# Performance work log

Hardware: AMD Instinct MI355X
Metric: run time of the kernel (lower is better)

Reference implementation:

```python
import jax, jax.numpy as jnp
import numpy as np

N, E = 50000, 150000
IN, HID, LAT, EF, HE = 16, 32, 16, 8, 128


def _p(k, shape, fan_in):
    return jax.random.normal(k, shape, jnp.float32) / np.float32(np.sqrt(fan_in))


def setup_inputs() -> dict:
    key = jax.random.key(0)
    ks = jax.random.split(key, 32)
    inp = {
        "x": jax.random.normal(ks[0], (N, IN), jnp.float32),
        "edge_index": jax.random.randint(ks[1], (2, E), 0, N, dtype=jnp.int64),
        "edge_attr": jax.random.uniform(ks[2], (E, EF), jnp.float32),
    }
    # per-conv params: edge-MLP (w1,b1,w2,b2), root weight, bias
    dims = {"c1": (IN, HID), "c2": (HID, HID), "cmu": (HID, LAT), "clv": (HID, LAT)}
    i = 3
    for name, (din, dout) in dims.items():
        inp[f"{name}_w1"] = _p(ks[i], (EF, HE), EF)
        inp[f"{name}_b1"] = jnp.zeros((HE,), jnp.float32)
        inp[f"{name}_w2"] = _p(ks[i + 1], (HE, din * dout), HE)
        inp[f"{name}_b2"] = jnp.zeros((din * dout,), jnp.float32)
        inp[f"{name}_root"] = _p(ks[i + 2], (din, dout), din)
        inp[f"{name}_bias"] = jnp.zeros((dout,), jnp.float32)
        i += 3
    return inp


def _nnconv(x, src, dst, ea, w1, b1, w2, b2, root, bias, din, dout, mean):
    # edge MLP -> per-edge weight matrix [E, din, dout]
    h = jax.nn.relu(ea @ w1 + b1)
    W = (h @ w2 + b2).reshape(-1, din, dout)
    # gather source features, per-edge matmul, scatter-reduce to targets
    msg = jnp.einsum('ei,eio->eo', x[src], W)  # [E, dout]
    agg = jax.ops.segment_sum(msg, dst, num_segments=x.shape[0])
    if mean:
        cnt = jax.ops.segment_sum(jnp.ones((dst.shape[0],), x.dtype), dst,
                                  num_segments=x.shape[0])
        agg = agg / jnp.maximum(cnt, 1.0)[:, None]
    return agg + x @ root + bias


def reference(x, edge_index, edge_attr,
              c1_w1, c1_b1, c1_w2, c1_b2, c1_root, c1_bias,
              c2_w1, c2_b1, c2_w2, c2_b2, c2_root, c2_bias,
              cmu_w1, cmu_b1, cmu_w2, cmu_b2, cmu_root, cmu_bias,
              clv_w1, clv_b1, clv_w2, clv_b2, clv_root, clv_bias):
    src, dst = edge_index[0], edge_index[1]
    h = jax.nn.relu(_nnconv(x, src, dst, edge_attr, c1_w1, c1_b1, c1_w2, c1_b2,
                            c1_root, c1_bias, IN, HID, True))
    h = jax.nn.relu(_nnconv(h, src, dst, edge_attr, c2_w1, c2_b1, c2_w2, c2_b2,
                            c2_root, c2_bias, HID, HID, True))
    mu = _nnconv(h, src, dst, edge_attr, cmu_w1, cmu_b1, cmu_w2, cmu_b2,
                 cmu_root, cmu_bias, HID, LAT, False)
    logvar = _nnconv(h, src, dst, edge_attr, clv_w1, clv_b1, clv_w2, clv_b2,
                     clv_root, clv_bias, HID, LAT, False)
    return mu, logvar
```

## Files before the change

kernel.cpp:

```cpp
#include <hip/hip_runtime.h>

typedef __attribute__((ext_vector_type(8))) _Float16 half8;
typedef __attribute__((ext_vector_type(4))) _Float16 half4v;
typedef __attribute__((ext_vector_type(2))) _Float16 half2v;
typedef __attribute__((ext_vector_type(4))) float f32x4;

constexpr int NN  = 50000;
constexpr int NE  = 150000;
constexpr int IN  = 16;
constexpr int HID = 32;
constexpr int LAT = 16;
constexpr int EF  = 8;
constexpr int HE  = 128;
constexpr int NTILE = NE / 16;
constexpr int HSTR  = HE + 2;

constexpr int SCB = 256;
constexpr int NSB = (NN + SCB - 1) / SCB;

union XU {
  half2v h2[4];
  half8  h8;
  _Float16 h[8];
};

__global__ void count_kernel(const int* __restrict__ dst, int* __restrict__ cnt) {
  int e = blockIdx.x * blockDim.x + threadIdx.x;
  if (e < NE) atomicAdd(&cnt[dst[e]], 1);
}

__launch_bounds__(SCB)
__global__ void scan1(const int* __restrict__ cnt, int* __restrict__ bsum) {
  __shared__ int sdata[SCB];
  const int i = blockIdx.x * SCB + threadIdx.x;
  sdata[threadIdx.x] = (i < NN) ? cnt[i] : 0;
  __syncthreads();
  for (int off = SCB / 2; off > 0; off >>= 1) {
    if (threadIdx.x < off) sdata[threadIdx.x] += sdata[threadIdx.x + off];
    __syncthreads();
  }
  if (threadIdx.x == 0) bsum[blockIdx.x] = sdata[0];
}

__launch_bounds__(SCB)
__global__ void scan2(int* __restrict__ bsum) {
  __shared__ int sdata[SCB];
  const int t = threadIdx.x;
  const int v = (t < NSB) ? bsum[t] : 0;
  sdata[t] = v;
  __syncthreads();
  for (int off = 1; off < SCB; off <<= 1) {
    int u = (t >= off) ? sdata[t - off] : 0;
    __syncthreads();
    sdata[t] += u;
    __syncthreads();
  }
  if (t < NSB) bsum[t] = sdata[t] - v;
}

__launch_bounds__(SCB)
__global__ void scan3(const int* __restrict__ cnt, const int* __restrict__ bsum,
                      int* __restrict__ rowptr, int* __restrict__ wptr) {
  __shared__ int sdata[SCB];
  const int i = blockIdx.x * SCB + threadIdx.x;
  const int t = threadIdx.x;
  const int v = (i < NN) ? cnt[i] : 0;
  sdata[t] = v;
  __syncthreads();
  for (int off = 1; off < SCB; off <<= 1) {
    int u = (t >= off) ? sdata[t - off] : 0;
    __syncthreads();
    sdata[t] += u;
    __syncthreads();
  }
  const int excl = sdata[t] - v + bsum[blockIdx.x];
  if (i < NN) {
    rowptr[i] = excl;
    wptr[i]   = excl;
  }
  if (i == NN - 1) rowptr[NN] = NE;
}

__global__ void fill_kernel(const int* __restrict__ dst, int* __restrict__ wptr,
                            int* __restrict__ epos) {
  int e = blockIdx.x * blockDim.x + threadIdx.x;
  if (e < NE) epos[e] = atomicAdd(&wptr[dst[e]], 1);
}

__global__ void swizzle_kernel(const float* __restrict__ w2, const float* __restrict__ b2,
                               const float* __restrict__ w1,
                               _Float16* __restrict__ w2h, float* __restrict__ w1t,
                               int DIN_, int DOUT_) {
  int idx = blockIdx.x * blockDim.x + threadIdx.x;
  if (idx < HE * EF) {
    int kk = idx / EF, i = idx % EF;
    w1t[idx] = w1[i * HE + kk];
  }
  int tot = HSTR * DIN_ * DOUT_;
  if (idx >= tot) return;
  int i  = idx % DIN_;
  int o  = (idx / DIN_) % DOUT_;
  int kk = idx / (DIN_ * DOUT_);
  float v = 0.0f;
  if (kk < HE)       v = w2[(size_t)kk * DIN_ * DOUT_ + i * DOUT_ + o];
  else if (kk == HE) v = b2[i * DOUT_ + o];
  w2h[idx] = (_Float16)v;
}

template <int DIN, int DOUT, bool DUAL>
__launch_bounds__(128)
__global__ void nnconv_mfma(const float* __restrict__ xin,
                            const int*   __restrict__ src,
                            const float* __restrict__ ea,
                            const float* __restrict__ w1tA,
                            const float* __restrict__ b1A,
                            const float* __restrict__ w1tB,
                            const float* __restrict__ b1B,
                            const _Float16* __restrict__ w2hA,
                            const _Float16* __restrict__ w2hB,
                            const int*   __restrict__ epos,
                            _Float16* __restrict__ msgA,
                            _Float16* __restrict__ msgB)
{
  constexpr int KKSTEP  = 32 / DIN;
  constexpr int CHS     = 8 / KKSTEP;
  constexpr int BSTRIDE = KKSTEP * DOUT * DIN;
  constexpr int HS      = 136;
  constexpr int TILES   = 4;

  __shared__ _Float16 h_s[128 * HS];

  const int tid = threadIdx.x;
  const int eb  = blockIdx.x * 128;

  float eav[EF];
  {
    const int e = eb + tid;
    float4 v0 = make_float4(0.f, 0.f, 0.f, 0.f), v1 = v0;
    if (e < NE) {
      const float4* p = (const float4*)(ea + (size_t)e * EF);
      v0 = p[0]; v1 = p[1];
    }
    eav[0] = v0.x; eav[1] = v0.y; eav[2] = v0.z; eav[3] = v0.w;
    eav[4] = v1.x; eav[5] = v1.y; eav[6] = v1.z; eav[7] = v1.w;
  }

  auto build_h = [&](const float* __restrict__ w1t, const float* __restrict__ b1) {
#pragma unroll 1
    for (int c = 0; c < 16; c++) {
      const float4 bq0 = *(const float4*)&b1[c * 8];
      const float4 bq1 = *(const float4*)&b1[c * 8 + 4];
      const float bk[8] = {bq0.x, bq0.y, bq0.z, bq0.w, bq1.x, bq1.y, bq1.z, bq1.w};
      XU hr;
#pragma unroll
      for (int j = 0; j < 8; j++) {
        const int kk = c * 8 + j;
        const float4 wa = *(const float4*)&w1t[kk * EF];
        const float4 wb = *(const float4*)&w1t[kk * EF + 4];
        float hv = bk[j];
        hv = fmaf(eav[0], wa.x, hv); hv = fmaf(eav[1], wa.y, hv);
        hv = fmaf(eav[2], wa.z, hv); hv = fmaf(eav[3], wa.w, hv);
        hv = fmaf(eav[4], wb.x, hv); hv = fmaf(eav[5], wb.y, hv);
        hv = fmaf(eav[6], wb.z, hv); hv = fmaf(eav[7], wb.w, hv);
        hv = fmaxf(hv, 0.0f);
        hr.h[j] = (_Float16)hv;
      }
      *(half8*)&h_s[tid * HS + c * 8] = hr.h8;
    }
  };

  build_h(w1tA, b1A);
  __syncthreads();

  const int wave = tid >> 6;
  const int lane = tid & 63;
  const int m = lane & 15, q = lane >> 4;
  const int i0 = (q * 8) % DIN;
  const int kq = (q * 8) / DIN;
  const int tg0 = blockIdx.x * 8 + wave * TILES;

  XU xv[TILES];
#pragma unroll
  for (int t = 0; t < TILES; t++) {
    const int tg = tg0 + t;
    if (tg < NTILE) {
      const int s = src[tg * 16 + m];
      const float4* xp = (const float4*)(xin + (size_t)s * DIN + i0);
      const float4 a = xp[0], b = xp[1];
      xv[t].h2[0] = (half2v){(_Float16)a.x, (_Float16)a.y};
      xv[t].h2[1] = (half2v){(_Float16)a.z, (_Float16)a.w};
      xv[t].h2[2] = (half2v){(_Float16)b.x, (_Float16)b.y};
      xv[t].h2[3] = (half2v){(_Float16)b.z, (_Float16)b.w};
    } else {
#pragma unroll
      for (int j = 0; j < 4; j++) xv[t].h2[j] = (half2v){(_Float16)0.f, (_Float16)0.f};
    }
  }

  f32x4 acc[TILES][2];
#pragma unroll
  for (int t = 0; t < TILES; t++)
#pragma unroll
    for (int f = 0; f < 2; f++) acc[t][f] = (f32x4){0.f, 0.f, 0.f, 0.f};

  int hrow[TILES];
#pragma unroll
  for (int t = 0; t < TILES; t++) hrow[t] = wave * 64 + t * 16 + m;

  auto make_af = [&](const XU& xvt, _Float16 hv) -> XU {
    const half2v hb = (half2v){hv, hv};
    XU af;
#pragma unroll
    for (int j = 0; j < 4; j++) af.h2[j] = xvt.h2[j] * hb;
    return af;
  };

  if constexpr (DUAL) {
    auto run_pass = [&](const _Float16* __restrict__ bp, const int f) {
#pragma unroll 1
      for (int c = 0; c < 16; c++) {
        XU hc[TILES];
#pragma unroll
        for (int t = 0; t < TILES; t++)
          hc[t].h8 = *(const half8*)&h_s[hrow[t] * HS + c * 8];
#pragma unroll
        for (int s = 0; s < CHS; s++) {
          const half8 bf = *(const half8*)(bp + (size_t)(c * CHS + s) * BSTRIDE);
#pragma unroll
          for (int t = 0; t < TILES; t++) {
            _Float16 hv;
            if (DIN == 32) hv = hc[t].h[s];
            else {
              const _Float16 h0 = hc[t].h[2 * s], h1 = hc[t].h[2 * s + 1];
              hv = kq ? h1 : h0;
            }
            const XU af = make_af(xv[t], hv);
            acc[t][f] = __builtin_amdgcn_mfma_f32_16x16x32_f16(af.h8, bf,
                                                               acc[t][f], 0, 0, 0);
          }
        }
      }
      {
        const half8 bf = *(const half8*)(bp + (size_t)(128 / KKSTEP) * BSTRIDE);
#pragma unroll
        for (int t = 0; t < TILES; t++) {
          XU af;
          if (DIN == 32) af = xv[t];
          else {
#pragma unroll
            for (int j = 0; j < 4; j++)
              af.h2[j] = kq ? (half2v){(_Float16)0.f, (_Float16)0.f} : xv[t].h2[j];
          }
          acc[t][f] = __builtin_amdgcn_mfma_f32_16x16x32_f16(af.h8, bf,
                                                             acc[t][f], 0, 0, 0);
        }
      }
    };

    const _Float16* bpA = w2hA + (size_t)(kq * DOUT + m) * DIN + i0;
    const _Float16* bpB = w2hB + (size_t)(kq * DOUT + m) * DIN + i0;
    run_pass(bpA, 0);
    __syncthreads();
    build_h(w1tB, b1B);
    __syncthreads();
    run_pass(bpB, 1);
  } else {
    const _Float16* bp0 = w2hA + (size_t)(kq * DOUT + 0 + m) * DIN + i0;
    const _Float16* bp1 = w2hA + (size_t)(kq * DOUT + 16 + m) * DIN + i0;
#pragma unroll 1
    for (int c = 0; c < 16; c++) {
      XU hc[TILES];
#pragma unroll
      for (int t = 0; t < TILES; t++)
        hc[t].h8 = *(const half8*)&h_s[hrow[t] * HS + c * 8];
#pragma unroll
      for (int s = 0; s < CHS; s++) {
        const half8 bf0 = *(const half8*)(bp0 + (size_t)(c * CHS + s) * BSTRIDE);
        const half8 bf1 = *(const half8*)(bp1 + (size_t)(c * CHS + s) * BSTRIDE);
#pragma unroll
        for (int t = 0; t < TILES; t++) {
          _Float16 hv;
          if (DIN == 32) hv = hc[t].h[s];
          else {
            const _Float16 h0 = hc[t].h[2 * s], h1 = hc[t].h[2 * s + 1];
            hv = kq ? h1 : h0;
          }
          const XU af = make_af(xv[t], hv);
          acc[t][0] = __builtin_amdgcn_mfma_f32_16x16x32_f16(af.h8, bf0,
                                                             acc[t][0], 0, 0, 0);
          acc[t][1] = __builtin_amdgcn_mfma_f32_16x16x32_f16(af.h8, bf1,
                                                             acc[t][1], 0, 0, 0);
        }
      }
    }
    {
      const half8 bf0 = *(const half8*)(bp0 + (size_t)(128 / KKSTEP) * BSTRIDE);
      const half8 bf1 = *(const half8*)(bp1 + (size_t)(128 / KKSTEP) * BSTRIDE);
#pragma unroll
      for (int t = 0; t < TILES; t++) {
        XU af;
        if (DIN == 32) af = xv[t];
        else {
#pragma unroll
          for (int j = 0; j < 4; j++)
            af.h2[j] = kq ? (half2v){(_Float16)0.f, (_Float16)0.f} : xv[t].h2[j];
        }
        acc[t][0] = __builtin_amdgcn_mfma_f32_16x16x32_f16(af.h8, bf0,
                                                           acc[t][0], 0, 0, 0);
        acc[t][1] = __builtin_amdgcn_mfma_f32_16x16x32_f16(af.h8, bf1,
                                                           acc[t][1], 0, 0, 0);
      }
    }
  }

#pragma unroll
  for (int t = 0; t < TILES; t++) {
    const int tg = tg0 + t;
    if (tg < NTILE) {
      const int ebase = tg * 16 + q * 4;
      const int4 ep = *(const int4*)(epos + ebase);
      const int pr[4] = {ep.x, ep.y, ep.z, ep.w};
      if (DUAL) {
#pragma unroll
        for (int r = 0; r < 4; r++) {
          msgA[(size_t)pr[r] * DOUT + m] = (_Float16)acc[t][0][r];
          msgB[(size_t)pr[r] * DOUT + m] = (_Float16)acc[t][1][r];
        }
      } else {
#pragma unroll
        for (int f = 0; f < 2; f++)
#pragma unroll
          for (int r = 0; r < 4; r++)
            msgA[(size_t)pr[r] * DOUT + f * 16 + m] = (_Float16)acc[t][f][r];
      }
    }
  }
}

template <int DIN, int DOUT, bool MEAN, bool RELU>
__launch_bounds__(256)
__global__ void finish_kernel(const _Float16* __restrict__ msg,
                              const int* __restrict__ rowptr,
                              const float* __restrict__ xin,
                              const float* __restrict__ root,
                              const float* __restrict__ bias,
                              float* __restrict__ out) {
  constexpr int TPN = DOUT / 4;
  const int gid = blockIdx.x * 256 + threadIdx.x;
  const int n = gid / TPN, sub = gid % TPN;
  if (n >= NN) return;
  const int o0 = sub * 4;

  const int r0 = rowptr[n], r1 = rowptr[n + 1];
  float ax = 0.f, ay = 0.f, az = 0.f, aw = 0.f;
  for (int idx = r0; idx < r1; idx++) {
    const half4v mv = *(const half4v*)(msg + (size_t)idx * DOUT + o0);
    ax += (float)mv.x; ay += (float)mv.y; az += (float)mv.z; aw += (float)mv.w;
  }
  const float inv = MEAN ? 1.0f / fmaxf((float)(r1 - r0), 1.0f) : 1.0f;
  float vx = ax * inv + bias[o0 + 0];
  float vy = ay * inv + bias[o0 + 1];
  float vz = az * inv + bias[o0 + 2];
  float vw = aw * inv + bias[o0 + 3];
#pragma unroll
  for (int i = 0; i < DIN; i++) {
    const float xi = xin[(size_t)n * DIN + i];
    const float4 rv = *(const float4*)(root + (size_t)i * DOUT + o0);
    vx = fmaf(xi, rv.x, vx); vy = fmaf(xi, rv.y, vy);
    vz = fmaf(xi, rv.z, vz); vw = fmaf(xi, rv.w, vw);
  }
  if (RELU) {
    vx = fmaxf(vx, 0.f); vy = fmaxf(vy, 0.f);
    vz = fmaxf(vz, 0.f); vw = fmaxf(vw, 0.f);
  }
  *(float4*)(out + (size_t)n * DOUT + o0) = make_float4(vx, vy, vz, vw);
}

template <int DIN>
__launch_bounds__(256)
__global__ void finish_dual(const _Float16* __restrict__ msgA,
                            const _Float16* __restrict__ msgB,
                            const int* __restrict__ rowptr,
                            const float* __restrict__ xin,
                            const float* __restrict__ rootA,
                            const float* __restrict__ biasA,
                            const float* __restrict__ rootB,
                            const float* __restrict__ biasB,
                            float* __restrict__ outA,
                            float* __restrict__ outB) {
  constexpr int TPN = LAT / 4;
  const int gid = blockIdx.x * 256 + threadIdx.x;
  const int n = gid / TPN, sub = gid % TPN;
  if (n >= NN) return;
  const int o0 = sub * 4;

  const int r0 = rowptr[n], r1 = rowptr[n + 1];
  float a0 = 0.f, a1 = 0.f, a2 = 0.f, a3 = 0.f;
  float b0 = 0.f, b1 = 0.f, b2 = 0.f, b3 = 0.f;
  for (int idx = r0; idx < r1; idx++) {
    const half4v ma = *(const half4v*)(msgA + (size_t)idx * LAT + o0);
    const half4v mb = *(const half4v*)(msgB + (size_t)idx * LAT + o0);
    a0 += (float)ma.x; a1 += (float)ma.y; a2 += (float)ma.z; a3 += (float)ma.w;
    b0 += (float)mb.x; b1 += (float)mb.y; b2 += (float)mb.z; b3 += (float)mb.w;
  }
  float va0 = a0 + biasA[o0 + 0], va1 = a1 + biasA[o0 + 1];
  float va2 = a2 + biasA[o0 + 2], va3 = a3 + biasA[o0 + 3];
  float vb0 = b0 + biasB[o0 + 0], vb1 = b1 + biasB[o0 + 1];
  float vb2 = b2 + biasB[o0 + 2], vb3 = b3 + biasB[o0 + 3];
#pragma unroll
  for (int i = 0; i < DIN; i++) {
    const float xi = xin[(size_t)n * DIN + i];
    const float4 ra = *(const float4*)(rootA + (size_t)i * LAT + o0);
    const float4 rb = *(const float4*)(rootB + (size_t)i * LAT + o0);
    va0 = fmaf(xi, ra.x, va0); va1 = fmaf(xi, ra.y, va1);
    va2 = fmaf(xi, ra.z, va2); va3 = fmaf(xi, ra.w, va3);
    vb0 = fmaf(xi, rb.x, vb0); vb1 = fmaf(xi, rb.y, vb1);
    vb2 = fmaf(xi, rb.z, vb2); vb3 = fmaf(xi, rb.w, vb3);
  }
  *(float4*)(outA + (size_t)n * LAT + o0) = make_float4(va0, va1, va2, va3);
  *(float4*)(outB + (size_t)n * LAT + o0) = make_float4(vb0, vb1, vb2, vb3);
}

extern "C" void kernel_launch(void* const* d_in, const int* in_sizes, int n_in,
                              void* d_out, int out_size, void* d_ws, size_t ws_size,
                              hipStream_t stream) {
  const float* x  = (const float*)d_in[0];
  const int*   ei = (const int*)d_in[1];
  const float* ea = (const float*)d_in[2];
  const int* src = ei;
  const int* dst = ei + NE;

  auto P = [&](int c, int j) -> const float* {
    return (const float*)d_in[3 + c * 6 + j];
  };

  float* h1  = (float*)d_ws;
  float* h2  = h1 + (size_t)NN * HID;
  _Float16* msg = (_Float16*)(h2 + (size_t)NN * HID);
  int* cnt    = (int*)(msg + (size_t)NE * 32);
  int* rowptr = cnt + NN;
  int* wptr   = rowptr + 50004;
  int* epos   = wptr + 50004;
  int* bsum   = epos + NE;
  _Float16* w2h_c1 = (_Float16*)(bsum + 256);
  _Float16* w2h_c2 = w2h_c1 + (size_t)HSTR * 32 * 16;
  _Float16* w2h_mu = w2h_c2 + (size_t)HSTR * 32 * 32;
  _Float16* w2h_lv = w2h_mu + (size_t)HSTR * 16 * 32;
  float* w1t_c1 = (float*)(w2h_lv + (size_t)HSTR * 16 * 32);
  float* w1t_c2 = w1t_c1 + HE * EF;
  float* w1t_mu = w1t_c2 + HE * EF;
  float* w1t_lv = w1t_mu + HE * EF;

  _Float16* msgA = msg;
  _Float16* msgB = msg + (size_t)NE * 16;

  float* out_mu = (float*)d_out;
  float* out_lv = out_mu + (size_t)NN * LAT;

  hipMemsetAsync(cnt, 0, (size_t)NN * sizeof(int), stream);
  count_kernel<<<dim3((NE + 255) / 256), dim3(256), 0, stream>>>(dst, cnt);
  scan1<<<dim3(NSB), dim3(SCB), 0, stream>>>(cnt, bsum);
  scan2<<<dim3(1), dim3(SCB), 0, stream>>>(bsum);
  scan3<<<dim3(NSB), dim3(SCB), 0, stream>>>(cnt, bsum, rowptr, wptr);
  fill_kernel<<<dim3((NE + 255) / 256), dim3(256), 0, stream>>>(dst, wptr, epos);

  {
    int t1 = HSTR * 16 * 32, t2 = HSTR * 32 * 32, t3 = HSTR * 32 * 16;
    swizzle_kernel<<<dim3((t1 + 255) / 256), dim3(256), 0, stream>>>(
        P(0, 2), P(0, 3), P(0, 0), w2h_c1, w1t_c1, IN, HID);
    swizzle_kernel<<<dim3((t2 + 255) / 256), dim3(256), 0, stream>>>(
        P(1, 2), P(1, 3), P(1, 0), w2h_c2, w1t_c2, HID, HID);
    swizzle_kernel<<<dim3((t3 + 255) / 256), dim3(256), 0, stream>>>(
        P(2, 2), P(2, 3), P(2, 0), w2h_mu, w1t_mu, HID, LAT);
    swizzle_kernel<<<dim3((t3 + 255) / 256), dim3(256), 0, stream>>>(
        P(3, 2), P(3, 3), P(3, 0), w2h_lv, w1t_lv, HID, LAT);
  }

  const dim3 egrid((NTILE + 7) / 8), eblk(128);

  nnconv_mfma<IN, HID, false><<<egrid, eblk, 0, stream>>>(
      x, src, ea, w1t_c1, P(0, 1), nullptr, nullptr, w2h_c1, nullptr,
      epos, msg, nullptr);
  finish_kernel<IN, HID, true, true>
      <<<dim3((NN * (HID / 4) + 255) / 256), dim3(256), 0, stream>>>(
          msg, rowptr, x, P(0, 4), P(0, 5), h1);

  nnconv_mfma<HID, HID, false><<<egrid, eblk, 0, stream>>>(
      h1, src, ea, w1t_c2, P(1, 1), nullptr, nullptr, w2h_c2, nullptr,
      epos, msg, nullptr);
  finish_kernel<HID, HID, true, true>
      <<<dim3((NN * (HID / 4) + 255) / 256), dim3(256), 0, stream>>>(
          msg, rowptr, h1, P(1, 4), P(1, 5), h2);

  nnconv_mfma<HID, LAT, true><<<egrid, eblk, 0, stream>>>(
      h2, src, ea, w1t_mu, P(2, 1), w1t_lv, P(3, 1), w2h_mu, w2h_lv,
      epos, msgA, msgB);
  finish_dual<HID>
      <<<dim3((NN * (LAT / 4) + 255) / 256), dim3(256), 0, stream>>>(
          msgA, msgB, rowptr, h2, P(2, 4), P(2, 5), P(3, 4), P(3, 5),
          out_mu, out_lv);
}
```

Before: 361.6 us.

## Split dual mu/logvar conv across waves instead of sequential passes

In the dual (mu/logvar) NNConv kernel, each 128-thread block now handles 64 edges, with wave 0 computing the mu branch and wave 1 the logvar branch at the same time. Before, both waves ran the mu pass, then a barrier, a rebuild of the hidden edge-MLP activations, another barrier, and the logvar pass. The change drops the mid-kernel barriers and the serial second build_h, and doubles the grid. The cost is that each edge's attributes and source features are loaded by both waves, and each wave now builds h for only 64 edges, which leaves half the LDS buffer unused.

```diff
diff --git a/kernel.cpp b/kernel.cpp
--- a/kernel.cpp
+++ b/kernel.cpp
@@ -127,15 +127,18 @@
   constexpr int BSTRIDE = KKSTEP * DOUT * DIN;
   constexpr int HS      = 136;
   constexpr int TILES   = 4;
+  constexpr int EDGES   = DUAL ? 64 : 128;
 
   __shared__ _Float16 h_s[128 * HS];
 
-  const int tid = threadIdx.x;
-  const int eb  = blockIdx.x * 128;
+  const int tid  = threadIdx.x;
+  const int wave = tid >> 6;
+  const int lane = tid & 63;
+  const int eb   = blockIdx.x * EDGES;
 
   float eav[EF];
   {
-    const int e = eb + tid;
+    const int e = eb + (DUAL ? lane : tid);
     float4 v0 = make_float4(0.f, 0.f, 0.f, 0.f), v1 = v0;
     if (e < NE) {
       const float4* p = (const float4*)(ea + (size_t)e * EF);
@@ -169,15 +172,18 @@
     }
   };
 
-  build_h(w1tA, b1A);
+  if constexpr (DUAL) {
+    build_h(wave == 0 ? w1tA : w1tB, wave == 0 ? b1A : b1B);
+  } else {
+    build_h(w1tA, b1A);
+  }
   __syncthreads();
 
-  const int wave = tid >> 6;
-  const int lane = tid & 63;
   const int m = lane & 15, q = lane >> 4;
   const int i0 = (q * 8) % DIN;
   const int kq = (q * 8) / DIN;
-  const int tg0 = blockIdx.x * 8 + wave * TILES;
+  const int tg0 = DUAL ? blockIdx.x * TILES
+                       : blockIdx.x * (2 * TILES) + wave * TILES;
 
   XU xv[TILES];
 #pragma unroll
@@ -197,12 +203,6 @@
     }
   }
 
-  f32x4 acc[TILES][2];
-#pragma unroll
-  for (int t = 0; t < TILES; t++)
-#pragma unroll
-    for (int f = 0; f < 2; f++) acc[t][f] = (f32x4){0.f, 0.f, 0.f, 0.f};
-
   int hrow[TILES];
 #pragma unroll
   for (int t = 0; t < TILES; t++) hrow[t] = wave * 64 + t * 16 + m;
@@ -216,55 +216,72 @@
   };
 
   if constexpr (DUAL) {
-    auto run_pass = [&](const _Float16* __restrict__ bp, const int f) {
+    f32x4 acc[TILES];
+#pragma unroll
+    for (int t = 0; t < TILES; t++) acc[t] = (f32x4){0.f, 0.f, 0.f, 0.f};
+
+    const _Float16* base = (wave == 0) ? w2hA : w2hB;
+    const _Float16* bp = base + (size_t)(kq * DOUT + m) * DIN + i0;
+
 #pragma unroll 1
-      for (int c = 0; c < 16; c++) {
-        XU hc[TILES];
-#pragma unroll
-        for (int t = 0; t < TILES; t++)
-          hc[t].h8 = *(const half8*)&h_s[hrow[t] * HS + c * 8];
-#pragma unroll
-        for (int s = 0; s < CHS; s++) {
-          const half8 bf = *(const half8*)(bp + (size_t)(c * CHS + s) * BSTRIDE);
-#pragma unroll
-          for (int t = 0; t < TILES; t++) {
-            _Float16 hv;
-            if (DIN == 32) hv = hc[t].h[s];
-            else {
-              const _Float16 h0 = hc[t].h[2 * s], h1 = hc[t].h[2 * s + 1];
-              hv = kq ? h1 : h0;
-            }
-            const XU af = make_af(xv[t], hv);
-            acc[t][f] = __builtin_amdgcn_mfma_f32_16x16x32_f16(af.h8, bf,
-                                                               acc[t][f], 0, 0, 0);
+    for (int c = 0; c < 16; c++) {
+      XU hc[TILES];
+#pragma unroll
+      for (int t = 0; t < TILES; t++)
+        hc[t].h8 = *(const half8*)&h_s[hrow[t] * HS + c * 8];
+#pragma unroll
+      for (int s = 0; s < CHS; s++) {
+        const half8 bf = *(const half8*)(bp + (size_t)(c * CHS + s) * BSTRIDE);
+#pragma unroll
+        for (int t = 0; t < TILES; t++) {
+          _Float16 hv;
+          if (DIN == 32) hv = hc[t].h[s];
+          else {
+            const _Float16 h0 = hc[t].h[2 * s], h1 = hc[t].h[2 * s + 1];
+            hv = kq ? h1 : h0;
           }
+          const XU af = make_af(xv[t], hv);
+          acc[t] = __builtin_amdgcn_mfma_f32_16x16x32_f16(af.h8, bf,
+                                                          acc[t], 0, 0, 0);
         }
       }
-      {
-        const half8 bf = *(const half8*)(bp + (size_t)(128 / KKSTEP) * BSTRIDE);
-#pragma unroll
-        for (int t = 0; t < TILES; t++) {
-          XU af;
-          if (DIN == 32) af = xv[t];
-          else {
-#pragma unroll
-            for (int j = 0; j < 4; j++)
-              af.h2[j] = kq ? (half2v){(_Float16)0.f, (_Float16)0.f} : xv[t].h2[j];
-          }
-          acc[t][f] = __builtin_amdgcn_mfma_f32_16x16x32_f16(af.h8, bf,
-                                                             acc[t][f], 0, 0, 0);
+    }
+    {
+      const half8 bf = *(const half8*)(bp + (size_t)(128 / KKSTEP) * BSTRIDE);
+#pragma unroll
+      for (int t = 0; t < TILES; t++) {
+        XU af;
+        if (DIN == 32) af = xv[t];
+        else {
+#pragma unroll
+          for (int j = 0; j < 4; j++)
+            af.h2[j] = kq ? (half2v){(_Float16)0.f, (_Float16)0.f} : xv[t].h2[j];
         }
-      }
-    };
-
-    const _Float16* bpA = w2hA + (size_t)(kq * DOUT + m) * DIN + i0;
-    const _Float16* bpB = w2hB + (size_t)(kq * DOUT + m) * DIN + i0;
-    run_pass(bpA, 0);
-    __syncthreads();
-    build_h(w1tB, b1B);
-    __syncthreads();
-    run_pass(bpB, 1);
+        acc[t] = __builtin_amdgcn_mfma_f32_16x16x32_f16(af.h8, bf,
+                                                        acc[t], 0, 0, 0);
+      }
+    }
+
+    _Float16* mout = (wave == 0) ? msgA : msgB;
+#pragma unroll
+    for (int t = 0; t < TILES; t++) {
+      const int tg = tg0 + t;
+      if (tg < NTILE) {
+        const int ebase = tg * 16 + q * 4;
+        const int4 ep = *(const int4*)(epos + ebase);
+        const int pr[4] = {ep.x, ep.y, ep.z, ep.w};
+#pragma unroll
+        for (int r = 0; r < 4; r++)
+          mout[(size_t)pr[r] * DOUT + m] = (_Float16)acc[t][r];
+      }
+    }
   } else {
+    f32x4 acc[TILES][2];
+#pragma unroll
+    for (int t = 0; t < TILES; t++)
+#pragma unroll
+      for (int f = 0; f < 2; f++) acc[t][f] = (f32x4){0.f, 0.f, 0.f, 0.f};
+
     const _Float16* bp0 = w2hA + (size_t)(kq * DOUT + 0 + m) * DIN + i0;
     const _Float16* bp1 = w2hA + (size_t)(kq * DOUT + 16 + m) * DIN + i0;
 #pragma unroll 1
@@ -311,22 +328,14 @@
                                                            acc[t][1], 0, 0, 0);
       }
     }
-  }
-
-#pragma unroll
-  for (int t = 0; t < TILES; t++) {
-    const int tg = tg0 + t;
-    if (tg < NTILE) {
-      const int ebase = tg * 16 + q * 4;
-      const int4 ep = *(const int4*)(epos + ebase);
-      const int pr[4] = {ep.x, ep.y, ep.z, ep.w};
-      if (DUAL) {
-#pragma unroll
-        for (int r = 0; r < 4; r++) {
-          msgA[(size_t)pr[r] * DOUT + m] = (_Float16)acc[t][0][r];
-          msgB[(size_t)pr[r] * DOUT + m] = (_Float16)acc[t][1][r];
-        }
-      } else {
+
+#pragma unroll
+    for (int t = 0; t < TILES; t++) {
+      const int tg = tg0 + t;
+      if (tg < NTILE) {
+        const int ebase = tg * 16 + q * 4;
+        const int4 ep = *(const int4*)(epos + ebase);
+        const int pr[4] = {ep.x, ep.y, ep.z, ep.w};
 #pragma unroll
         for (int f = 0; f < 2; f++)
 #pragma unroll
@@ -477,6 +486,7 @@
   }
 
   const dim3 egrid((NTILE + 7) / 8), eblk(128);
+  const dim3 dgrid((NTILE + 3) / 4);
 
   nnconv_mfma<IN, HID, false><<<egrid, eblk, 0, stream>>>(
       x, src, ea, w1t_c1, P(0, 1), nullptr, nullptr, w2h_c1, nullptr,
@@ -492,7 +502,7 @@
       <<<dim3((NN * (HID / 4) + 255) / 256), dim3(256), 0, stream>>>(
           msg, rowptr, h1, P(1, 4), P(1, 5), h2);
 
-  nnconv_mfma<HID, LAT, true><<<egrid, eblk, 0, stream>>>(
+  nnconv_mfma<HID, LAT, true><<<dgrid, eblk, 0, stream>>>(
       h2, src, ea, w1t_mu, P(2, 1), w1t_lv, P(3, 1), w2h_mu, w2h_lv,
       epos, msgA, msgB);
   finish_dual<HID>
```

Result: slower. 379.5 us (+5.0%).

## Split edge-MLP hidden dimension across two blocks with partial message buffers

Applied to the files above, without the earlier changes.

Adds a second grid dimension that splits the 128-wide edge-MLP hidden reduction into two halves, each block building only 64 hidden units in a smaller shared tile and writing its partial messages to a separate buffer. The finish kernels then sum the two partial message buffers while aggregating. This doubles the block count and halves the shared memory per block, aiming at more occupancy and parallelism in the MFMA kernels. In exchange, the edge features and source rows are loaded twice, and the message write and read traffic doubles.

```diff
diff --git a/kernel.cpp b/kernel.cpp
--- a/kernel.cpp
+++ b/kernel.cpp
@@ -125,13 +125,17 @@
   constexpr int KKSTEP  = 32 / DIN;
   constexpr int CHS     = 8 / KKSTEP;
   constexpr int BSTRIDE = KKSTEP * DOUT * DIN;
-  constexpr int HS      = 136;
+  constexpr int HS      = 72;
+  constexpr int CPB     = 8;
   constexpr int TILES   = 4;
 
   __shared__ _Float16 h_s[128 * HS];
 
-  const int tid = threadIdx.x;
-  const int eb  = blockIdx.x * 128;
+  const int tid  = threadIdx.x;
+  const int wave = tid >> 6;
+  const int lane = tid & 63;
+  const int eb   = blockIdx.x * 128;
+  const int yh   = blockIdx.y;
 
   float eav[EF];
   {
@@ -147,14 +151,15 @@
 
   auto build_h = [&](const float* __restrict__ w1t, const float* __restrict__ b1) {
 #pragma unroll 1
-    for (int c = 0; c < 16; c++) {
-      const float4 bq0 = *(const float4*)&b1[c * 8];
-      const float4 bq1 = *(const float4*)&b1[c * 8 + 4];
+    for (int c = 0; c < CPB; c++) {
+      const int kk0 = yh * 64 + c * 8;
+      const float4 bq0 = *(const float4*)&b1[kk0];
+      const float4 bq1 = *(const float4*)&b1[kk0 + 4];
       const float bk[8] = {bq0.x, bq0.y, bq0.z, bq0.w, bq1.x, bq1.y, bq1.z, bq1.w};
       XU hr;
 #pragma unroll
       for (int j = 0; j < 8; j++) {
-        const int kk = c * 8 + j;
+        const int kk = kk0 + j;
         const float4 wa = *(const float4*)&w1t[kk * EF];
         const float4 wb = *(const float4*)&w1t[kk * EF + 4];
         float hv = bk[j];
@@ -172,8 +177,6 @@
   build_h(w1tA, b1A);
   __syncthreads();
 
-  const int wave = tid >> 6;
-  const int lane = tid & 63;
   const int m = lane & 15, q = lane >> 4;
   const int i0 = (q * 8) % DIN;
   const int kq = (q * 8) / DIN;
@@ -197,12 +200,6 @@
     }
   }
 
-  f32x4 acc[TILES][2];
-#pragma unroll
-  for (int t = 0; t < TILES; t++)
-#pragma unroll
-    for (int f = 0; f < 2; f++) acc[t][f] = (f32x4){0.f, 0.f, 0.f, 0.f};
-
   int hrow[TILES];
 #pragma unroll
   for (int t = 0; t < TILES; t++) hrow[t] = wave * 64 + t * 16 + m;
@@ -215,17 +212,26 @@
     return af;
   };
 
+  const int stepbase = yh * CPB * CHS;
+
   if constexpr (DUAL) {
+    f32x4 acc[TILES][2];
+#pragma unroll
+    for (int t = 0; t < TILES; t++)
+#pragma unroll
+      for (int f = 0; f < 2; f++) acc[t][f] = (f32x4){0.f, 0.f, 0.f, 0.f};
+
     auto run_pass = [&](const _Float16* __restrict__ bp, const int f) {
 #pragma unroll 1
-      for (int c = 0; c < 16; c++) {
+      for (int c = 0; c < CPB; c++) {
         XU hc[TILES];
 #pragma unroll
         for (int t = 0; t < TILES; t++)
           hc[t].h8 = *(const half8*)&h_s[hrow[t] * HS + c * 8];
 #pragma unroll
         for (int s = 0; s < CHS; s++) {
-          const half8 bf = *(const half8*)(bp + (size_t)(c * CHS + s) * BSTRIDE);
+          const half8 bf =
+              *(const half8*)(bp + (size_t)(stepbase + c * CHS + s) * BSTRIDE);
 #pragma unroll
           for (int t = 0; t < TILES; t++) {
             _Float16 hv;
@@ -240,7 +246,7 @@
           }
         }
       }
-      {
+      if (yh == 0) {
         const half8 bf = *(const half8*)(bp + (size_t)(128 / KKSTEP) * BSTRIDE);
 #pragma unroll
         for (int t = 0; t < TILES; t++) {
@@ -264,19 +270,44 @@
     build_h(w1tB, b1B);
     __syncthreads();
     run_pass(bpB, 1);
+
+    _Float16* moutA = msgA + (size_t)yh * NE * DOUT;
+    _Float16* moutB = msgB + (size_t)yh * NE * DOUT;
+#pragma unroll
+    for (int t = 0; t < TILES; t++) {
+      const int tg = tg0 + t;
+      if (tg < NTILE) {
+        const int ebase = tg * 16 + q * 4;
+        const int4 ep = *(const int4*)(epos + ebase);
+        const int pr[4] = {ep.x, ep.y, ep.z, ep.w};
+#pragma unroll
+        for (int r = 0; r < 4; r++) {
+          moutA[(size_t)pr[r] * DOUT + m] = (_Float16)acc[t][0][r];
+          moutB[(size_t)pr[r] * DOUT + m] = (_Float16)acc[t][1][r];
+        }
+      }
+    }
   } else {
+    f32x4 acc[TILES][2];
+#pragma unroll
+    for (int t = 0; t < TILES; t++)
+#pragma unroll
+      for (int f = 0; f < 2; f++) acc[t][f] = (f32x4){0.f, 0.f, 0.f, 0.f};
+
     const _Float16* bp0 = w2hA + (size_t)(kq * DOUT + 0 + m) * DIN + i0;
     const _Float16* bp1 = w2hA + (size_t)(kq * DOUT + 16 + m) * DIN + i0;
 #pragma unroll 1
-    for (int c = 0; c < 16; c++) {
+    for (int c = 0; c < CPB; c++) {
       XU hc[TILES];
 #pragma unroll
       for (int t = 0; t < TILES; t++)
         hc[t].h8 = *(const half8*)&h_s[hrow[t] * HS + c * 8];
 #pragma unroll
       for (int s = 0; s < CHS; s++) {
-        const half8 bf0 = *(const half8*)(bp0 + (size_t)(c * CHS + s) * BSTRIDE);
-        const half8 bf1 = *(const half8*)(bp1 + (size_t)(c * CHS + s) * BSTRIDE);
+        const half8 bf0 =
+            *(const half8*)(bp0 + (size_t)(stepbase + c * CHS + s) * BSTRIDE);
+        const half8 bf1 =
+            *(const half8*)(bp1 + (size_t)(stepbase + c * CHS + s) * BSTRIDE);
 #pragma unroll
         for (int t = 0; t < TILES; t++) {
           _Float16 hv;
@@ -293,7 +324,7 @@
         }
       }
     }
-    {
+    if (yh == 0) {
       const half8 bf0 = *(const half8*)(bp0 + (size_t)(128 / KKSTEP) * BSTRIDE);
       const half8 bf1 = *(const half8*)(bp1 + (size_t)(128 / KKSTEP) * BSTRIDE);
 #pragma unroll
@@ -311,27 +342,20 @@
                                                            acc[t][1], 0, 0, 0);
       }
     }
-  }
-
-#pragma unroll
-  for (int t = 0; t < TILES; t++) {
-    const int tg = tg0 + t;
-    if (tg < NTILE) {
-      const int ebase = tg * 16 + q * 4;
-      const int4 ep = *(const int4*)(epos + ebase);
-      const int pr[4] = {ep.x, ep.y, ep.z, ep.w};
-      if (DUAL) {
-#pragma unroll
-        for (int r = 0; r < 4; r++) {
-          msgA[(size_t)pr[r] * DOUT + m] = (_Float16)acc[t][0][r];
-          msgB[(size_t)pr[r] * DOUT + m] = (_Float16)acc[t][1][r];
-        }
-      } else {
+
+    _Float16* mout = msgA + (size_t)yh * NE * DOUT;
+#pragma unroll
+    for (int t = 0; t < TILES; t++) {
+      const int tg = tg0 + t;
+      if (tg < NTILE) {
+        const int ebase = tg * 16 + q * 4;
+        const int4 ep = *(const int4*)(epos + ebase);
+        const int pr[4] = {ep.x, ep.y, ep.z, ep.w};
 #pragma unroll
         for (int f = 0; f < 2; f++)
 #pragma unroll
           for (int r = 0; r < 4; r++)
-            msgA[(size_t)pr[r] * DOUT + f * 16 + m] = (_Float16)acc[t][f][r];
+            mout[(size_t)pr[r] * DOUT + f * 16 + m] = (_Float16)acc[t][f][r];
       }
     }
   }
@@ -350,12 +374,15 @@
   const int n = gid / TPN, sub = gid % TPN;
   if (n >= NN) return;
   const int o0 = sub * 4;
+  const _Float16* msg1 = msg + (size_t)NE * DOUT;
 
   const int r0 = rowptr[n], r1 = rowptr[n + 1];
   float ax = 0.f, ay = 0.f, az = 0.f, aw = 0.f;
   for (int idx = r0; idx < r1; idx++) {
-    const half4v mv = *(const half4v*)(msg + (size_t)idx * DOUT + o0);
-    ax += (float)mv.x; ay += (float)mv.y; az += (float)mv.z; aw += (float)mv.w;
+    const half4v m0 = *(const half4v*)(msg  + (size_t)idx * DOUT + o0);
+    const half4v m1 = *(const half4v*)(msg1 + (size_t)idx * DOUT + o0);
+    ax += (float)m0.x + (float)m1.x; ay += (float)m0.y + (float)m1.y;
+    az += (float)m0.z + (float)m1.z; aw += (float)m0.w + (float)m1.w;
   }
   const float inv = MEAN ? 1.0f / fmaxf((float)(r1 - r0), 1.0f) : 1.0f;
   float vx = ax * inv + bias[o0 + 0];
@@ -393,15 +420,21 @@
   const int n = gid / TPN, sub = gid % TPN;
   if (n >= NN) return;
   const int o0 = sub * 4;
+  const _Float16* msgA1 = msgA + (size_t)NE * LAT;
+  const _Float16* msgB1 = msgB + (size_t)NE * LAT;
 
   const int r0 = rowptr[n], r1 = rowptr[n + 1];
   float a0 = 0.f, a1 = 0.f, a2 = 0.f, a3 = 0.f;
   float b0 = 0.f, b1 = 0.f, b2 = 0.f, b3 = 0.f;
   for (int idx = r0; idx < r1; idx++) {
-    const half4v ma = *(const half4v*)(msgA + (size_t)idx * LAT + o0);
-    const half4v mb = *(const half4v*)(msgB + (size_t)idx * LAT + o0);
-    a0 += (float)ma.x; a1 += (float)ma.y; a2 += (float)ma.z; a3 += (float)ma.w;
-    b0 += (float)mb.x; b1 += (float)mb.y; b2 += (float)mb.z; b3 += (float)mb.w;
+    const half4v ma0 = *(const half4v*)(msgA  + (size_t)idx * LAT + o0);
+    const half4v ma1 = *(const half4v*)(msgA1 + (size_t)idx * LAT + o0);
+    const half4v mb0 = *(const half4v*)(msgB  + (size_t)idx * LAT + o0);
+    const half4v mb1 = *(const half4v*)(msgB1 + (size_t)idx * LAT + o0);
+    a0 += (float)ma0.x + (float)ma1.x; a1 += (float)ma0.y + (float)ma1.y;
+    a2 += (float)ma0.z + (float)ma1.z; a3 += (float)ma0.w + (float)ma1.w;
+    b0 += (float)mb0.x + (float)mb1.x; b1 += (float)mb0.y + (float)mb1.y;
+    b2 += (float)mb0.z + (float)mb1.z; b3 += (float)mb0.w + (float)mb1.w;
   }
   float va0 = a0 + biasA[o0 + 0], va1 = a1 + biasA[o0 + 1];
   float va2 = a2 + biasA[o0 + 2], va3 = a3 + biasA[o0 + 3];
@@ -437,7 +470,7 @@
   float* h1  = (float*)d_ws;
   float* h2  = h1 + (size_t)NN * HID;
   _Float16* msg = (_Float16*)(h2 + (size_t)NN * HID);
-  int* cnt    = (int*)(msg + (size_t)NE * 32);
+  int* cnt    = (int*)(msg + (size_t)NE * 64);
   int* rowptr = cnt + NN;
   int* wptr   = rowptr + 50004;
   int* epos   = wptr + 50004;
@@ -452,7 +485,7 @@
   float* w1t_lv = w1t_mu + HE * EF;
 
   _Float16* msgA = msg;
-  _Float16* msgB = msg + (size_t)NE * 16;
+  _Float16* msgB = msg + (size_t)NE * 32;
 
   float* out_mu = (float*)d_out;
   float* out_lv = out_mu + (size_t)NN * LAT;
@@ -476,21 +509,21 @@
         P(3, 2), P(3, 3), P(3, 0), w2h_lv, w1t_lv, HID, LAT);
   }
 
-  const dim3 egrid((NTILE + 7) / 8), eblk(128);
+  const dim3 egrid((NTILE + 7) / 8, 2), eblk(128);
 
   nnconv_mfma<IN, HID, false><<<egrid, eblk, 0, stream>>>(
       x, src, ea, w1t_c1, P(0, 1), nullptr, nullptr, w2h_c1, nullptr,
-      epos, msg, nullptr);
+      epos, msgA, nullptr);
   finish_kernel<IN, HID, true, true>
       <<<dim3((NN * (HID / 4) + 255) / 256), dim3(256), 0, stream>>>(
-          msg, rowptr, x, P(0, 4), P(0, 5), h1);
+          msgA, rowptr, x, P(0, 4), P(0, 5), h1);
 
   nnconv_mfma<HID, HID, false><<<egrid, eblk, 0, stream>>>(
       h1, src, ea, w1t_c2, P(1, 1), nullptr, nullptr, w2h_c2, nullptr,
-      epos, msg, nullptr);
+      epos, msgA, nullptr);
   finish_kernel<HID, HID, true, true>
       <<<dim3((NN * (HID / 4) + 255) / 256), dim3(256), 0, stream>>>(
-          msg, rowptr, h1, P(1, 4), P(1, 5), h2);
+          msgA, rowptr, h1, P(1, 4), P(1, 5), h2);
 
   nnconv_mfma<HID, LAT, true><<<egrid, eblk, 0, stream>>>(
       h2, src, ea, w1t_mu, P(2, 1), w1t_lv, P(3, 1), w2h_mu, w2h_lv,
```

After: 391.3 us. +8.2%, slower.

## Interleave hidden-activation build with MFMA loop using double-buffered chunk LDS

Applied to the files above, without the earlier changes.

Instead of building the full 128x128 edge-MLP hidden tile in shared memory before the MFMA loop, each 8-wide chunk of hidden units is computed per iteration into a small double-buffered LDS area, and both convs of the dual path are built and consumed in the same loop. This shrinks LDS from about 34KB to a few KB, which could raise occupancy. Interleaving VALU hidden-unit computation with MFMA work lets the two overlap. The cost is one barrier per chunk instead of one or three overall, and the dual path now keeps more live registers because both accumulators and both hidden chunks are active at once.

```diff
diff --git a/kernel.cpp b/kernel.cpp
--- a/kernel.cpp
+++ b/kernel.cpp
@@ -125,13 +125,15 @@
   constexpr int KKSTEP  = 32 / DIN;
   constexpr int CHS     = 8 / KKSTEP;
   constexpr int BSTRIDE = KKSTEP * DOUT * DIN;
-  constexpr int HS      = 136;
   constexpr int TILES   = 4;
-
-  __shared__ _Float16 h_s[128 * HS];
-
-  const int tid = threadIdx.x;
-  const int eb  = blockIdx.x * 128;
+  constexpr int NTAB    = DUAL ? 2 : 1;
+
+  __shared__ _Float16 h_s[2 * NTAB * 128 * 8];
+
+  const int tid  = threadIdx.x;
+  const int wave = tid >> 6;
+  const int lane = tid & 63;
+  const int eb   = blockIdx.x * 128;
 
   float eav[EF];
   {
@@ -145,35 +147,30 @@
     eav[4] = v1.x; eav[5] = v1.y; eav[6] = v1.z; eav[7] = v1.w;
   }
 
-  auto build_h = [&](const float* __restrict__ w1t, const float* __restrict__ b1) {
-#pragma unroll 1
-    for (int c = 0; c < 16; c++) {
-      const float4 bq0 = *(const float4*)&b1[c * 8];
-      const float4 bq1 = *(const float4*)&b1[c * 8 + 4];
-      const float bk[8] = {bq0.x, bq0.y, bq0.z, bq0.w, bq1.x, bq1.y, bq1.z, bq1.w};
-      XU hr;
-#pragma unroll
-      for (int j = 0; j < 8; j++) {
-        const int kk = c * 8 + j;
-        const float4 wa = *(const float4*)&w1t[kk * EF];
-        const float4 wb = *(const float4*)&w1t[kk * EF + 4];
-        float hv = bk[j];
-        hv = fmaf(eav[0], wa.x, hv); hv = fmaf(eav[1], wa.y, hv);
-        hv = fmaf(eav[2], wa.z, hv); hv = fmaf(eav[3], wa.w, hv);
-        hv = fmaf(eav[4], wb.x, hv); hv = fmaf(eav[5], wb.y, hv);
-        hv = fmaf(eav[6], wb.z, hv); hv = fmaf(eav[7], wb.w, hv);
-        hv = fmaxf(hv, 0.0f);
-        hr.h[j] = (_Float16)hv;
-      }
-      *(half8*)&h_s[tid * HS + c * 8] = hr.h8;
-    }
+  auto build_chunk = [&](const float* __restrict__ w1t,
+                         const float* __restrict__ b1,
+                         int c, _Float16* __restrict__ dst) {
+    const int kk0 = c * 8;
+    const float4 bq0 = *(const float4*)&b1[kk0];
+    const float4 bq1 = *(const float4*)&b1[kk0 + 4];
+    const float bk[8] = {bq0.x, bq0.y, bq0.z, bq0.w, bq1.x, bq1.y, bq1.z, bq1.w};
+    XU hr;
+#pragma unroll
+    for (int j = 0; j < 8; j++) {
+      const int kk = kk0 + j;
+      const float4 wa = *(const float4*)&w1t[kk * EF];
+      const float4 wb = *(const float4*)&w1t[kk * EF + 4];
+      float hv = bk[j];
+      hv = fmaf(eav[0], wa.x, hv); hv = fmaf(eav[1], wa.y, hv);
+      hv = fmaf(eav[2], wa.z, hv); hv = fmaf(eav[3], wa.w, hv);
+      hv = fmaf(eav[4], wb.x, hv); hv = fmaf(eav[5], wb.y, hv);
+      hv = fmaf(eav[6], wb.z, hv); hv = fmaf(eav[7], wb.w, hv);
+      hv = fmaxf(hv, 0.0f);
+      hr.h[j] = (_Float16)hv;
+    }
+    *(half8*)&dst[tid * 8] = hr.h8;
   };
 
-  build_h(w1tA, b1A);
-  __syncthreads();
-
-  const int wave = tid >> 6;
-  const int lane = tid & 63;
   const int m = lane & 15, q = lane >> 4;
   const int i0 = (q * 8) % DIN;
   const int kq = (q * 8) / DIN;
@@ -215,101 +212,82 @@
     return af;
   };
 
-  if constexpr (DUAL) {
-    auto run_pass = [&](const _Float16* __restrict__ bp, const int f) {
+  const _Float16* bp0;
+  const _Float16* bp1;
+  if (DUAL) {
+    bp0 = w2hA + (size_t)(kq * DOUT + m) * DIN + i0;
+    bp1 = w2hB + (size_t)(kq * DOUT + m) * DIN + i0;
+  } else {
+    bp0 = w2hA + (size_t)(kq * DOUT + 0 + m) * DIN + i0;
+    bp1 = w2hA + (size_t)(kq * DOUT + 16 + m) * DIN + i0;
+  }
+
 #pragma unroll 1
-      for (int c = 0; c < 16; c++) {
-        XU hc[TILES];
-#pragma unroll
-        for (int t = 0; t < TILES; t++)
-          hc[t].h8 = *(const half8*)&h_s[hrow[t] * HS + c * 8];
-#pragma unroll
-        for (int s = 0; s < CHS; s++) {
-          const half8 bf = *(const half8*)(bp + (size_t)(c * CHS + s) * BSTRIDE);
-#pragma unroll
-          for (int t = 0; t < TILES; t++) {
-            _Float16 hv;
-            if (DIN == 32) hv = hc[t].h[s];
-            else {
-              const _Float16 h0 = hc[t].h[2 * s], h1 = hc[t].h[2 * s + 1];
-              hv = kq ? h1 : h0;
-            }
-            const XU af = make_af(xv[t], hv);
-            acc[t][f] = __builtin_amdgcn_mfma_f32_16x16x32_f16(af.h8, bf,
-                                                               acc[t][f], 0, 0, 0);
+  for (int c = 0; c < 16; c++) {
+    _Float16* buf = &h_s[(size_t)(c & 1) * NTAB * 128 * 8];
+    build_chunk(w1tA, b1A, c, buf);
+    if (DUAL) build_chunk(w1tB, b1B, c, buf + 128 * 8);
+    __syncthreads();
+
+    XU hc0[TILES], hc1[TILES];
+#pragma unroll
+    for (int t = 0; t < TILES; t++)
+      hc0[t].h8 = *(const half8*)&buf[hrow[t] * 8];
+    if (DUAL) {
+#pragma unroll
+      for (int t = 0; t < TILES; t++)
+        hc1[t].h8 = *(const half8*)&buf[128 * 8 + hrow[t] * 8];
+    }
+
+#pragma unroll
+    for (int s = 0; s < CHS; s++) {
+      const half8 bf0 = *(const half8*)(bp0 + (size_t)(c * CHS + s) * BSTRIDE);
+      const half8 bf1 = *(const half8*)(bp1 + (size_t)(c * CHS + s) * BSTRIDE);
+#pragma unroll
+      for (int t = 0; t < TILES; t++) {
+        _Float16 hv0;
+        if (DIN == 32) hv0 = hc0[t].h[s];
+        else {
+          const _Float16 h0 = hc0[t].h[2 * s], h1 = hc0[t].h[2 * s + 1];
+          hv0 = kq ? h1 : h0;
+        }
+        const XU af0 = make_af(xv[t], hv0);
+        acc[t][0] = __builtin_amdgcn_mfma_f32_16x16x32_f16(af0.h8, bf0,
+                                                           acc[t][0], 0, 0, 0);
+        if (DUAL) {
+          _Float16 hv1;
+          if (DIN == 32) hv1 = hc1[t].h[s];
+          else {
+            const _Float16 h0 = hc1[t].h[2 * s], h1 = hc1[t].h[2 * s + 1];
+            hv1 = kq ? h1 : h0;
           }
-        }
-      }
-      {
-        const half8 bf = *(const half8*)(bp + (size_t)(128 / KKSTEP) * BSTRIDE);
-#pragma unroll
-        for (int t = 0; t < TILES; t++) {
-          XU af;
-          if (DIN == 32) af = xv[t];
-          else {
-#pragma unroll
-            for (int j = 0; j < 4; j++)
-              af.h2[j] = kq ? (half2v){(_Float16)0.f, (_Float16)0.f} : xv[t].h2[j];
-          }
-          acc[t][f] = __builtin_amdgcn_mfma_f32_16x16x32_f16(af.h8, bf,
-                                                             acc[t][f], 0, 0, 0);
-        }
-      }
-    };
-
-    const _Float16* bpA = w2hA + (size_t)(kq * DOUT + m) * DIN + i0;
-    const _Float16* bpB = w2hB + (size_t)(kq * DOUT + m) * DIN + i0;
-    run_pass(bpA, 0);
-    __syncthreads();
-    build_h(w1tB, b1B);
-    __syncthreads();
-    run_pass(bpB, 1);
-  } else {
-    const _Float16* bp0 = w2hA + (size_t)(kq * DOUT + 0 + m) * DIN + i0;
-    const _Float16* bp1 = w2hA + (size_t)(kq * DOUT + 16 + m) * DIN + i0;
-#pragma unroll 1
-    for (int c = 0; c < 16; c++) {
-      XU hc[TILES];
-#pragma unroll
-      for (int t = 0; t < TILES; t++)
-        hc[t].h8 = *(const half8*)&h_s[hrow[t] * HS + c * 8];
-#pragma unroll
-      for (int s = 0; s < CHS; s++) {
-        const half8 bf0 = *(const half8*)(bp0 + (size_t)(c * CHS + s) * BSTRIDE);
-        const half8 bf1 = *(const half8*)(bp1 + (size_t)(c * CHS + s) * BSTRIDE);
-#pragma unroll
-        for (int t = 0; t < TILES; t++) {
-          _Float16 hv;
-          if (DIN == 32) hv = hc[t].h[s];
-          else {
-            const _Float16 h0 = hc[t].h[2 * s], h1 = hc[t].h[2 * s + 1];
-            hv = kq ? h1 : h0;
-          }
-          const XU af = make_af(xv[t], hv);
-          acc[t][0] = __builtin_amdgcn_mfma_f32_16x16x32_f16(af.h8, bf0,
-                                                             acc[t][0], 0, 0, 0);
-          acc[t][1] = __builtin_amdgcn_mfma_f32_16x16x32_f16(af.h8, bf1,
+          const XU af1 = make_af(xv[t], hv1);
+          acc[t][1] = __builtin_amdgcn_mfma_f32_16x16x32_f16(af1.h8, bf1,
+                                                             acc[t][1], 0, 0, 0);
+        } else {
+          acc[t][1] = __builtin_amdgcn_mfma_f32_16x16x32_f16(af0.h8, bf1,
                                                              acc[t][1], 0, 0, 0);
         }
       }
     }
-    {
-      const half8 bf0 = *(const half8*)(bp0 + (size_t)(128 / KKSTEP) * BSTRIDE);
-      const half8 bf1 = *(const half8*)(bp1 + (size_t)(128 / KKSTEP) * BSTRIDE);
-#pragma unroll
-      for (int t = 0; t < TILES; t++) {
-        XU af;
-        if (DIN == 32) af = xv[t];
-        else {
-#pragma unroll
-          for (int j = 0; j < 4; j++)
-            af.h2[j] = kq ? (half2v){(_Float16)0.f, (_Float16)0.f} : xv[t].h2[j];
-        }
-        acc[t][0] = __builtin_amdgcn_mfma_f32_16x16x32_f16(af.h8, bf0,
-                                                           acc[t][0], 0, 0, 0);
-        acc[t][1] = __builtin_amdgcn_mfma_f32_16x16x32_f16(af.h8, bf1,
-                                                           acc[t][1], 0, 0, 0);
+  }
+
+  {
+    const half8 bf0 = *(const half8*)(bp0 + (size_t)(128 / KKSTEP) * BSTRIDE);
+    const half8 bf1 = *(const half8*)(bp1 + (size_t)(128 / KKSTEP) * BSTRIDE);
+#pragma unroll
+    for (int t = 0; t < TILES; t++) {
+      XU af;
+      if (DIN == 32) af = xv[t];
+      else {
+#pragma unroll
+        for (int j = 0; j < 4; j++)
+          af.h2[j] = kq ? (half2v){(_Float16)0.f, (_Float16)0.f} : xv[t].h2[j];
       }
+      acc[t][0] = __builtin_amdgcn_mfma_f32_16x16x32_f16(af.h8, bf0,
+                                                         acc[t][0], 0, 0, 0);
+      acc[t][1] = __builtin_amdgcn_mfma_f32_16x16x32_f16(af.h8, bf1,
+                                                         acc[t][1], 0, 0, 0);
     }
   }
 
```

Result: faster. 343.6 us (-5.0%).
